# Kernel optimization log

Measured on AMD Instinct MI355X. Metric: run time of the kernel, lower is better.

## Reference

```python
import jax, jax.numpy as jnp
import numpy as np

ATT_DIM = 512
HEADS = 8
HEAD_DIM = ATT_DIM // HEADS
D_IN = 512
LEFT_MASK = 256
RIGHT_MASK = 0
LARGE = 1e30


def pos_encoding(S, d):
    # Transformer-XL sinusoid table over relative positions S-1 .. -(S-1), length 2S-1.
    inv_freq = (1.0 / (10000.0 ** (np.arange(0, d, 2.0) / d))).astype(np.float32)
    pos = jnp.arange(S - 1, -S, -1, dtype=jnp.float32)          # [2S-1]
    ang = pos[:, None] * jnp.asarray(inv_freq)[None, :]          # [2S-1, d/2]
    # concat([sin, cos], -1) on a trailing singleton -> interleaved sin/cos per frequency
    return jnp.stack([jnp.sin(ang), jnp.cos(ang)], axis=-1).reshape(2 * S - 1, d)


def rel_shift(x):
    # x: [B, N, S, 2S-1] -> [B, N, S, S] with out[i, j] = x[i, S-1 - i + j]
    B, N, S, L = x.shape
    x = jnp.pad(x, ((0, 0), (0, 0), (0, 0), (1, 0)))             # [B,N,S,L+1]
    x = x.reshape(B, N, L + 1, S)[:, :, 1:, :]                   # [B,N,L,S]
    x = x.reshape(B, N, S, L)
    return x[:, :, :, :S]


def setup_inputs() -> dict:
    key = jax.random.key(0)
    ks = jax.random.split(key, 9)
    B, S, D = 2, 2048, D_IN
    scale = 0.02
    return {
        "x": jax.random.normal(ks[0], (B, S, D), dtype=jnp.float32),
        "Wq": jax.random.normal(ks[1], (D, ATT_DIM), dtype=jnp.float32) * scale,
        "b_con": jax.random.normal(ks[2], (ATT_DIM,), dtype=jnp.float32) * scale,
        "b_rel": jax.random.normal(ks[3], (ATT_DIM,), dtype=jnp.float32) * scale,
        "Wk": jax.random.normal(ks[4], (D, ATT_DIM), dtype=jnp.float32) * scale,
        "Wkr": jax.random.normal(ks[5], (D_IN, ATT_DIM), dtype=jnp.float32) * scale,
        "Wv": jax.random.normal(ks[6], (D, ATT_DIM), dtype=jnp.float32) * scale,
        "bv": jax.random.normal(ks[7], (ATT_DIM,), dtype=jnp.float32) * scale,
        "x_len": jax.random.randint(ks[8], (B,), 1, S + 1).astype(jnp.int32),
    }


def reference(x, Wq, b_con, b_rel, Wk, Wkr, Wv, bv, x_len):
    B, S, D = x.shape
    N, Dh = HEADS, HEAD_DIM

    # content/relative query share the kernel (TiedDense) with separate biases
    q_lin = jnp.einsum('bsd,de->bse', x, Wq)
    q_con = (q_lin + b_con).reshape(B, S, N, Dh)
    q_rel = (q_lin + b_rel).reshape(B, S, N, Dh)
    k_con = jnp.einsum('bsd,de->bse', x, Wk).reshape(B, S, N, Dh)

    content_energy = jnp.einsum('bind,bjnd->bnij', q_con, k_con)  # [B,N,S,S]

    pos_emb = pos_encoding(S, D_IN)                               # [2S-1, D]
    k_rel = (pos_emb @ Wkr).reshape(2 * S - 1, N, Dh)
    relative_energy = jnp.einsum('bind,jnd->bnij', q_rel, k_rel)  # [B,N,S,2S-1]
    relative_energy = rel_shift(relative_energy)                  # [B,N,S,S]

    energy = (content_energy + relative_energy) / jnp.sqrt(jnp.float32(Dh))

    # sequence mask over keys (broadcast [B,1,1,S]) * banded mask (band_part)
    j = jnp.arange(S)
    seq_mask = (j[None, :] < x_len[:, None]).astype(jnp.float32)[:, None, None, :]
    i = jnp.arange(S)[:, None]
    band = ((i - j[None, :] <= LEFT_MASK) & (j[None, :] - i <= RIGHT_MASK)).astype(jnp.float32)
    mask = seq_mask * band[None, None, :, :]

    masked_energy = energy - (1.0 - mask) * LARGE
    attention = jax.nn.softmax(masked_energy, axis=-1)

    v = (jnp.einsum('bsd,de->bse', x, Wv) + bv).reshape(B, S, N, Dh)
    context = jnp.einsum('bnij,bjnd->bind', attention, v).reshape(B, S, N * Dh)
    return context
```

## Files before the change

### kernel.cpp

```cpp
#include <hip/hip_runtime.h>
#include <math.h>

#define S_ 2048
#define NH 8
#define DH 64
#define RSTRIDE 264
#define LP 72

typedef __attribute__((ext_vector_type(8))) short short8;
typedef __attribute__((ext_vector_type(4))) float f32x4;
typedef unsigned short ushort_t;

__device__ __forceinline__ short bf16r(float x) {
    union { float f; unsigned u; } v; v.f = x;
    unsigned r = v.u + 0x7fffu + ((v.u >> 16) & 1u);
    return (short)(r >> 16);
}
__device__ __forceinline__ float b2f(ushort_t h) {
    union { float f; unsigned u; } v; v.u = ((unsigned)h) << 16; return v.f;
}

__global__ __launch_bounds__(256) void prep_kernel(
    const float* __restrict__ Wq, const float* __restrict__ Wk,
    const float* __restrict__ Wv, const float* __restrict__ Wkr,
    ushort_t* __restrict__ WTq, ushort_t* __restrict__ WTk,
    ushort_t* __restrict__ WTv, ushort_t* __restrict__ WTkr,
    ushort_t* __restrict__ pos)
{
    const int widx = blockIdx.z;
    const int t = threadIdx.x;
    if (widx == 4) {
        const int base = blockIdx.y * 8 + blockIdx.x;
        const float C = -0.051905126482615036f;
        const int f = t;
#pragma unroll
        for (int rep = 0; rep < 6; ++rep) {
            const int r = base + rep * 64;
            unsigned pk = 0;
            if (r <= 256) {
                float ang = (float)r * exp2f(C * (float)f);
                unsigned s = (unsigned)(ushort_t)bf16r(sinf(ang));
                unsigned c = (unsigned)(ushort_t)bf16r(cosf(ang));
                pk = s | (c << 16);
            }
            ((unsigned*)pos)[(size_t)r * 256 + f] = pk;
        }
        return;
    }
    const float* W = (widx == 0) ? Wq : (widx == 1) ? Wk : (widx == 2) ? Wv : Wkr;
    ushort_t* WT   = (widx == 0) ? WTq : (widx == 1) ? WTk : (widx == 2) ? WTv : WTkr;
    const int k0 = blockIdx.x * 64, n0 = blockIdx.y * 64;
    __shared__ __align__(16) ushort_t T[64][72];
    const int srow = t >> 2, sc0 = (t & 3) * 16;
    const float* src = &W[(size_t)(k0 + srow) * 512 + n0 + sc0];
#pragma unroll
    for (int u = 0; u < 16; ++u) T[sc0 + u][srow] = (ushort_t)bf16r(src[u]);
    __syncthreads();
    ushort_t* dst = &WT[(size_t)(n0 + srow) * 512 + k0 + sc0];
    *(short8*)dst       = *(const short8*)&T[srow][sc0];
    *(short8*)(dst + 8) = *(const short8*)&T[srow][sc0 + 8];
}

__global__ __launch_bounds__(256) void qkv_gemm(
    const float* __restrict__ x,
    const ushort_t* __restrict__ WTq, const ushort_t* __restrict__ WTk,
    const ushort_t* __restrict__ WTv,
    const ushort_t* __restrict__ pos, const ushort_t* __restrict__ WTkr,
    const float* __restrict__ b_con, const float* __restrict__ b_rel,
    const float* __restrict__ bv,
    ushort_t* __restrict__ qcon, ushort_t* __restrict__ qrel,
    ushort_t* __restrict__ kout, ushort_t* __restrict__ vT,
    ushort_t* __restrict__ krel)
{
    const int widx = blockIdx.y >> 3;
    const int tid = threadIdx.x, lane = tid & 63, w = tid >> 6;
    const int quad = lane >> 4, l16 = lane & 15;

    __shared__ __align__(16) ushort_t A_lds[128][40];
    __shared__ __align__(16) ushort_t B_lds[64][40];

    f32x4 acc[2][4];
#pragma unroll
    for (int mt = 0; mt < 2; ++mt)
#pragma unroll
        for (int nt = 0; nt < 4; ++nt) acc[mt][nt] = (f32x4){0.f, 0.f, 0.f, 0.f};

    const int arow = tid >> 1, ak0 = (tid & 1) * 16;
    const int brow = tid >> 2, bk0 = (tid & 3) * 8;

    if (widx < 2) {
        const int m0 = blockIdx.x * 128;
        const int n0 = (blockIdx.y & 7) * 64;
        const ushort_t* WT = (widx == 0) ? WTq : WTk;

        for (int k0 = 0; k0 < 512; k0 += 32) {
            const float* xs = &x[(size_t)(m0 + arow) * 512 + k0 + ak0];
            ushort_t t16[16];
#pragma unroll
            for (int u = 0; u < 16; ++u) t16[u] = (ushort_t)bf16r(xs[u]);
            *(short8*)&A_lds[arow][ak0]     = *(short8*)&t16[0];
            *(short8*)&A_lds[arow][ak0 + 8] = *(short8*)&t16[8];
            *(short8*)&B_lds[brow][bk0] =
                *(const short8*)&WT[(size_t)(n0 + brow) * 512 + k0 + bk0];
            __syncthreads();
            short8 a0 = *(const short8*)&A_lds[w * 32 + l16][quad * 8];
            short8 a1 = *(const short8*)&A_lds[w * 32 + 16 + l16][quad * 8];
#pragma unroll
            for (int nt = 0; nt < 4; ++nt) {
                short8 bb = *(const short8*)&B_lds[nt * 16 + l16][quad * 8];
                acc[0][nt] = __builtin_amdgcn_mfma_f32_16x16x32_bf16(a0, bb, acc[0][nt], 0, 0, 0);
                acc[1][nt] = __builtin_amdgcn_mfma_f32_16x16x32_bf16(a1, bb, acc[1][nt], 0, 0, 0);
            }
            __syncthreads();
        }

#pragma unroll
        for (int nt = 0; nt < 4; ++nt) {
            const int col = n0 + nt * 16 + l16;
            float bc = 0.f, br = 0.f;
            if (widx == 0) { bc = b_con[col]; br = b_rel[col]; }
#pragma unroll
            for (int mt = 0; mt < 2; ++mt) {
#pragma unroll
                for (int reg = 0; reg < 4; ++reg) {
                    const size_t m = (size_t)(m0 + w * 32 + mt * 16 + quad * 4 + reg);
                    const float val = acc[mt][nt][reg];
                    if (widx == 0) {
                        qcon[m * 512 + col] = (ushort_t)bf16r((val + bc) * 0.125f);
                        qrel[m * 512 + col] = (ushort_t)bf16r((val + br) * 0.125f);
                    } else {
                        kout[m * 512 + col] = (ushort_t)bf16r(val);
                    }
                }
            }
        }
    } else if (widx == 2) {
        const int vb = (blockIdx.y & 7) * 32 + blockIdx.x;
        const int m0d = (vb & 3) * 128;
        const int n0j = (vb >> 2) * 64;

        for (int k0 = 0; k0 < 512; k0 += 32) {
            *(short8*)&A_lds[arow][ak0] =
                *(const short8*)&WTv[(size_t)(m0d + arow) * 512 + k0 + ak0];
            *(short8*)&A_lds[arow][ak0 + 8] =
                *(const short8*)&WTv[(size_t)(m0d + arow) * 512 + k0 + ak0 + 8];
            const float* xs = &x[(size_t)(n0j + brow) * 512 + k0 + bk0];
            ushort_t t8[8];
#pragma unroll
            for (int u = 0; u < 8; ++u) t8[u] = (ushort_t)bf16r(xs[u]);
            *(short8*)&B_lds[brow][bk0] = *(short8*)&t8[0];
            __syncthreads();
            short8 a0 = *(const short8*)&A_lds[w * 32 + l16][quad * 8];
            short8 a1 = *(const short8*)&A_lds[w * 32 + 16 + l16][quad * 8];
#pragma unroll
            for (int nt = 0; nt < 4; ++nt) {
                short8 bb = *(const short8*)&B_lds[nt * 16 + l16][quad * 8];
                acc[0][nt] = __builtin_amdgcn_mfma_f32_16x16x32_bf16(a0, bb, acc[0][nt], 0, 0, 0);
                acc[1][nt] = __builtin_amdgcn_mfma_f32_16x16x32_bf16(a1, bb, acc[1][nt], 0, 0, 0);
            }
            __syncthreads();
        }

        const int b = n0j >> 11;
#pragma unroll
        for (int mt = 0; mt < 2; ++mt) {
#pragma unroll
            for (int reg = 0; reg < 4; ++reg) {
                const int d = m0d + w * 32 + mt * 16 + quad * 4 + reg;
                const int n = d >> 6, dd = d & 63;
                const float bvv = bv[d];
#pragma unroll
                for (int nt = 0; nt < 4; ++nt) {
                    const int s = (n0j + nt * 16 + l16) & 2047;
                    vT[((size_t)((b * NH + n) * 64 + dd)) * 2048 + s] =
                        (ushort_t)bf16r(acc[mt][nt][reg] + bvv);
                }
            }
        }
    } else {
        if (blockIdx.x >= 24) return;
        const int m0 = (blockIdx.x >> 3) * 128;
        const int n0 = (blockIdx.x & 7) * 64;

        for (int k0 = 0; k0 < 512; k0 += 32) {
            const ushort_t* ps = &pos[(size_t)(m0 + arow) * 512 + k0 + ak0];
            *(short8*)&A_lds[arow][ak0]     = *(const short8*)ps;
            *(short8*)&A_lds[arow][ak0 + 8] = *(const short8*)(ps + 8);
            *(short8*)&B_lds[brow][bk0] =
                *(const short8*)&WTkr[(size_t)(n0 + brow) * 512 + k0 + bk0];
            __syncthreads();
            short8 a0 = *(const short8*)&A_lds[w * 32 + l16][quad * 8];
            short8 a1 = *(const short8*)&A_lds[w * 32 + 16 + l16][quad * 8];
#pragma unroll
            for (int nt = 0; nt < 4; ++nt) {
                short8 bb = *(const short8*)&B_lds[nt * 16 + l16][quad * 8];
                acc[0][nt] = __builtin_amdgcn_mfma_f32_16x16x32_bf16(a0, bb, acc[0][nt], 0, 0, 0);
                acc[1][nt] = __builtin_amdgcn_mfma_f32_16x16x32_bf16(a1, bb, acc[1][nt], 0, 0, 0);
            }
            __syncthreads();
        }

#pragma unroll
        for (int nt = 0; nt < 4; ++nt) {
            const int col = n0 + nt * 16 + l16;
#pragma unroll
            for (int mt = 0; mt < 2; ++mt)
#pragma unroll
                for (int reg = 0; reg < 4; ++reg) {
                    const size_t m = (size_t)(m0 + w * 32 + mt * 16 + quad * 4 + reg);
                    krel[m * 512 + col] = (ushort_t)bf16r(acc[mt][nt][reg]);
                }
        }
    }
}

__global__ __launch_bounds__(256) void rel_gemm(
    const ushort_t* __restrict__ qrel, const ushort_t* __restrict__ krel,
    const ushort_t* __restrict__ vT, ushort_t* __restrict__ R,
    float* __restrict__ vmean)
{
    const int tile = blockIdx.x, n = blockIdx.y, b = blockIdx.z;
    const int tid = threadIdx.x, lane = tid & 63, w = tid >> 6;
    const int quad = lane >> 4, l16 = lane & 15;

    __shared__ __align__(16) ushort_t A_lds[128][LP];
    __shared__ __align__(16) ushort_t B_lds[64][LP];

    if (tile == 16) {
        const int row = tid >> 2, seg = tid & 3;
        const ushort_t* src = &vT[((size_t)((b * NH + n) * 64 + row)) * 2048 + seg * 512];
        float sum = 0.f;
        for (int it = 0; it < 64; ++it) {
            short8 h = *(const short8*)(src + it * 8);
#pragma unroll
            for (int u = 0; u < 8; ++u) sum += b2f((ushort_t)h[u]);
        }
        float* scratch = (float*)A_lds;
        scratch[row * 4 + seg] = sum;
        __syncthreads();
        if (tid < 64) {
            float s = scratch[tid * 4] + scratch[tid * 4 + 1]
                    + scratch[tid * 4 + 2] + scratch[tid * 4 + 3];
            vmean[(size_t)b * 512 + n * 64 + tid] = s * (1.0f / (float)S_);
        }
        return;
    }

    const int i0 = tile * 128;
    {
        const int srow = tid >> 1, sc0 = (tid & 1) * 32;
        const ushort_t* src = &qrel[((size_t)b * S_ + i0 + srow) * 512 + n * 64 + sc0];
#pragma unroll
        for (int u = 0; u < 4; ++u)
            *(short8*)&A_lds[srow][sc0 + u * 8] = *(const short8*)(src + u * 8);
    }

    const size_t rbase = ((size_t)(b * NH + n) * S_ + i0) * RSTRIDE;
    const int srow2 = tid >> 2, sc2 = (tid & 3) * 16;

#pragma unroll 1
    for (int rc = 0; rc < 5; ++rc) {
        __syncthreads();
        {
            const ushort_t* src = &krel[(size_t)(rc * 64 + srow2) * 512 + n * 64 + sc2];
            *(short8*)&B_lds[srow2][sc2]     = *(const short8*)src;
            *(short8*)&B_lds[srow2][sc2 + 8] = *(const short8*)(src + 8);
        }
        __syncthreads();

        short8 a[2][2];
#pragma unroll
        for (int mt = 0; mt < 2; ++mt) {
            a[mt][0] = *(const short8*)&A_lds[w * 32 + mt * 16 + l16][quad * 8];
            a[mt][1] = *(const short8*)&A_lds[w * 32 + mt * 16 + l16][quad * 8 + 32];
        }
#pragma unroll
        for (int nt = 0; nt < 4; ++nt) {
            short8 b0 = *(const short8*)&B_lds[nt * 16 + l16][quad * 8];
            short8 b1 = *(const short8*)&B_lds[nt * 16 + l16][quad * 8 + 32];
            const int r = rc * 64 + nt * 16 + l16;
#pragma unroll
            for (int mt = 0; mt < 2; ++mt) {
                f32x4 s = (f32x4){0.f, 0.f, 0.f, 0.f};
                s = __builtin_amdgcn_mfma_f32_16x16x32_bf16(a[mt][0], b0, s, 0, 0, 0);
                s = __builtin_amdgcn_mfma_f32_16x16x32_bf16(a[mt][1], b1, s, 0, 0, 0);
                if (r < RSTRIDE) {
#pragma unroll
                    for (int reg = 0; reg < 4; ++reg) {
                        const int i = w * 32 + mt * 16 + quad * 4 + reg;
                        R[rbase + (size_t)i * RSTRIDE + r] = (ushort_t)bf16r(s[reg]);
                    }
                }
            }
        }
    }
}

__global__ __launch_bounds__(128) void attn_kernel(
    const ushort_t* __restrict__ qcon, const ushort_t* __restrict__ kbuf,
    const ushort_t* __restrict__ vT, const ushort_t* __restrict__ R,
    const float* __restrict__ vmean, const int* __restrict__ xlen_p,
    float* __restrict__ out)
{
    const int bx = blockIdx.x;
    const int tile = ((bx & 7) << 3) | (bx >> 3);
    const int n = blockIdx.y, b = blockIdx.z;
    const int i0 = tile * 32;
    const int tid = threadIdx.x, lane = tid & 63, w = tid >> 6;
    const int quad = lane >> 4, l16 = lane & 15;
    const int xlen = xlen_p[b];

    __shared__ __align__(16) ushort_t q_lds[32][LP];
    __shared__ __align__(16) ushort_t k_lds[64][LP];
    __shared__ __align__(16) ushort_t vT_lds[64][LP];
    __shared__ __align__(16) ushort_t p_lds[32][LP];

    {
        const int qr = tid >> 2, qc = (tid & 3) * 16;
        const ushort_t* src = &qcon[((size_t)b * S_ + i0 + qr) * 512 + n * 64 + qc];
        *(short8*)&q_lds[qr][qc]     = *(const short8*)src;
        *(short8*)&q_lds[qr][qc + 8] = *(const short8*)(src + 8);
    }

    f32x4 Oa[4];
#pragma unroll
    for (int nt = 0; nt < 4; ++nt) Oa[nt] = (f32x4){0.f, 0.f, 0.f, 0.f};
    float lpart[4] = {};

    const size_t rrowB = (size_t)(b * NH + n) * S_ * RSTRIDE;
    const size_t vTbase = (size_t)((b * NH + n) * 64) * 2048;
    const int srow = tid >> 1, sc0 = (tid & 1) * 32;
    const short8 z8 = {0, 0, 0, 0, 0, 0, 0, 0};

    short8 kr[4], vr[4], kn[4], vn[4];
    ushort_t rc_[16], rn_[16];

    auto issue = [&](int c, short8* kd, short8* vd, ushort_t* rd) {
        const int jc0 = i0 - 256 + c * 64;
        const int jg = jc0 + srow;
        const bool okk = (jg >= 0);
        const ushort_t* ks = &kbuf[((size_t)b * S_ + jg) * 512 + n * 64 + sc0];
        const ushort_t* vs = &vT[vTbase + (size_t)srow * 2048 + jc0 + sc0];
#pragma unroll
        for (int u = 0; u < 4; ++u) {
            kd[u] = okk ? *(const short8*)(ks + u * 8) : z8;
            const bool okv = (jc0 + sc0 + u * 8) >= 0;
            vd[u] = okv ? *(const short8*)(vs + u * 8) : z8;
        }
#pragma unroll
        for (int jt = 0; jt < 4; ++jt) {
#pragma unroll
            for (int reg = 0; reg < 4; ++reg) {
                const int i = i0 + w * 16 + quad * 4 + reg;
                const int j = jc0 + jt * 16 + l16;
                const int r = i - j;
                const bool valid = (j >= 0) && (j < xlen) && (r >= 0) && (r <= 256);
                rd[jt * 4 + reg] = valid ? R[rrowB + (size_t)i * RSTRIDE + r]
                                         : (ushort_t)0;
            }
        }
    };

    issue(0, kr, vr, rc_);

#pragma unroll 1
    for (int c = 0; c < 5; ++c) {
        const int jc0 = i0 - 256 + c * 64;
        __syncthreads();
#pragma unroll
        for (int u = 0; u < 4; ++u) {
            *(short8*)&k_lds[srow][sc0 + u * 8]  = kr[u];
            *(short8*)&vT_lds[srow][sc0 + u * 8] = vr[u];
        }
        if (c < 4) issue(c + 1, kn, vn, rn_);
        __syncthreads();

        short8 aq0 = *(const short8*)&q_lds[w * 16 + l16][quad * 8];
        short8 aq1 = *(const short8*)&q_lds[w * 16 + l16][quad * 8 + 32];
        f32x4 Sacc[4];
#pragma unroll
        for (int jt = 0; jt < 4; ++jt) {
            short8 bk0 = *(const short8*)&k_lds[jt * 16 + l16][quad * 8];
            short8 bk1 = *(const short8*)&k_lds[jt * 16 + l16][quad * 8 + 32];
            f32x4 s = (f32x4){0.f, 0.f, 0.f, 0.f};
            s = __builtin_amdgcn_mfma_f32_16x16x32_bf16(aq0, bk0, s, 0, 0, 0);
            s = __builtin_amdgcn_mfma_f32_16x16x32_bf16(aq1, bk1, s, 0, 0, 0);
            Sacc[jt] = s;
        }

#pragma unroll
        for (int jt = 0; jt < 4; ++jt) {
#pragma unroll
            for (int reg = 0; reg < 4; ++reg) {
                const int i = i0 + w * 16 + quad * 4 + reg;
                const int j = jc0 + jt * 16 + l16;
                const int r = i - j;
                const bool valid = (j >= 0) && (j < xlen) && (r >= 0) && (r <= 256);
                float e = valid ? __expf(Sacc[jt][reg] + b2f(rc_[jt * 4 + reg])) : 0.f;
                lpart[reg] += e;
                p_lds[w * 16 + quad * 4 + reg][jt * 16 + l16] = (ushort_t)bf16r(e);
            }
        }
        __syncthreads();

        short8 ap0 = *(const short8*)&p_lds[w * 16 + l16][quad * 8];
        short8 ap1 = *(const short8*)&p_lds[w * 16 + l16][quad * 8 + 32];
#pragma unroll
        for (int nt = 0; nt < 4; ++nt) {
            short8 bv0 = *(const short8*)&vT_lds[nt * 16 + l16][quad * 8];
            short8 bv1 = *(const short8*)&vT_lds[nt * 16 + l16][quad * 8 + 32];
            Oa[nt] = __builtin_amdgcn_mfma_f32_16x16x32_bf16(ap0, bv0, Oa[nt], 0, 0, 0);
            Oa[nt] = __builtin_amdgcn_mfma_f32_16x16x32_bf16(ap1, bv1, Oa[nt], 0, 0, 0);
        }

#pragma unroll
        for (int u = 0; u < 4; ++u) { kr[u] = kn[u]; vr[u] = vn[u]; }
#pragma unroll
        for (int u = 0; u < 16; ++u) rc_[u] = rn_[u];
    }

#pragma unroll
    for (int reg = 0; reg < 4; ++reg) {
#pragma unroll
        for (int off = 1; off < 16; off <<= 1)
            lpart[reg] += __shfl_xor(lpart[reg], off, 64);
    }

#pragma unroll
    for (int reg = 0; reg < 4; ++reg) {
        const int i = i0 + w * 16 + quad * 4 + reg;
        const bool dead = (i >= xlen + 256);
        const float linv = 1.0f / lpart[reg];
#pragma unroll
        for (int nt = 0; nt < 4; ++nt) {
            const int d = n * 64 + nt * 16 + l16;
            float val = dead ? vmean[(size_t)b * 512 + d] : Oa[nt][reg] * linv;
            out[((size_t)b * S_ + i) * 512 + d] = val;
        }
    }
}

extern "C" void kernel_launch(void* const* d_in, const int* in_sizes, int n_in,
                              void* d_out, int out_size, void* d_ws, size_t ws_size,
                              hipStream_t stream) {
    const float* x     = (const float*)d_in[0];
    const float* Wq    = (const float*)d_in[1];
    const float* b_con = (const float*)d_in[2];
    const float* b_rel = (const float*)d_in[3];
    const float* Wk    = (const float*)d_in[4];
    const float* Wkr   = (const float*)d_in[5];
    const float* Wv    = (const float*)d_in[6];
    const float* bv    = (const float*)d_in[7];
    const int*   xlen  = (const int*)d_in[8];
    float* out = (float*)d_out;

    float* ws = (float*)d_ws;
    float* vmean = ws;
    ushort_t* ub   = (ushort_t*)(vmean + 1024);
    ushort_t* R    = ub;
    ushort_t* qcon = R    + 8650752;
    ushort_t* kbuf = qcon + 2097152;
    ushort_t* vT   = kbuf + 2097152;
    ushort_t* qrel = vT   + 2097152;
    ushort_t* krel = qrel + 2097152;
    ushort_t* pos  = krel + 196608;
    ushort_t* WTq  = pos  + 196608;
    ushort_t* WTk  = WTq + 262144;
    ushort_t* WTv  = WTk + 262144;
    ushort_t* WTkr = WTv + 262144;

    prep_kernel<<<dim3(8, 8, 5), 256, 0, stream>>>(Wq, Wk, Wv, Wkr,
                                                   WTq, WTk, WTv, WTkr, pos);
    qkv_gemm<<<dim3(32, 25), 256, 0, stream>>>(x, WTq, WTk, WTv, pos, WTkr,
                                               b_con, b_rel, bv,
                                               qcon, qrel, kbuf, vT, krel);
    rel_gemm<<<dim3(17, 8, 2), 256, 0, stream>>>(qrel, krel, vT, R, vmean);
    attn_kernel<<<dim3(64, 8, 2), 128, 0, stream>>>(qcon, kbuf, vT, R, vmean,
                                                    xlen, out);
}
```

Measured before the change: 146.6 us.

## Fuse relative-position GEMM into attention kernel and compute value mean algebraically

Drops the separate rel_gemm kernel and its large global R buffer. Each attention block now computes its own 32x257 relative-energy band from qrel and krel into shared memory and reads it during softmax, instead of gathering scalars from global memory. The value mean used for fully masked rows is now computed as mean(x)·Wv + bv, with mean(x) produced in prep_kernel and the small GEMV run in spare qkv_gemm blocks. This cuts one launch and a large write/read round trip. In exchange the attention kernel does extra MFMA work and krel loads, uses more LDS (lower occupancy), and mean(x)·Wv in fp32 differs slightly from averaging the bf16 V values.

```diff
diff --git a/kernel.cpp b/kernel.cpp
--- a/kernel.cpp
+++ b/kernel.cpp
@@ -4,7 +4,6 @@
 #define S_ 2048
 #define NH 8
 #define DH 64
-#define RSTRIDE 264
 #define LP 72
 
 typedef __attribute__((ext_vector_type(8))) short short8;
@@ -21,14 +20,17 @@
 }
 
 __global__ __launch_bounds__(256) void prep_kernel(
+    const float* __restrict__ x,
     const float* __restrict__ Wq, const float* __restrict__ Wk,
     const float* __restrict__ Wv, const float* __restrict__ Wkr,
     ushort_t* __restrict__ WTq, ushort_t* __restrict__ WTk,
     ushort_t* __restrict__ WTv, ushort_t* __restrict__ WTkr,
-    ushort_t* __restrict__ pos)
+    ushort_t* __restrict__ pos, float* __restrict__ xbar)
 {
     const int widx = blockIdx.z;
     const int t = threadIdx.x;
+    __shared__ __align__(16) ushort_t T[64][72];
+
     if (widx == 4) {
         const int base = blockIdx.y * 8 + blockIdx.x;
         const float C = -0.051905126482615036f;
@@ -47,10 +49,24 @@
         }
         return;
     }
+    if (widx == 5) {
+        if (blockIdx.y >= 2) return;
+        const int b = blockIdx.y, e0 = blockIdx.x * 64;
+        const int el = t & 63, stripe = t >> 6;
+        const float* xs = &x[((size_t)b * S_ + stripe * 512) * 512 + e0 + el];
+        float sum = 0.f;
+        for (int s = 0; s < 512; ++s) sum += xs[(size_t)s * 512];
+        float* sc = (float*)T;
+        sc[stripe * 64 + el] = sum;
+        __syncthreads();
+        if (t < 64)
+            xbar[b * 512 + e0 + t] =
+                (sc[t] + sc[64 + t] + sc[128 + t] + sc[192 + t]) * (1.0f / 2048.f);
+        return;
+    }
     const float* W = (widx == 0) ? Wq : (widx == 1) ? Wk : (widx == 2) ? Wv : Wkr;
     ushort_t* WT   = (widx == 0) ? WTq : (widx == 1) ? WTk : (widx == 2) ? WTv : WTkr;
     const int k0 = blockIdx.x * 64, n0 = blockIdx.y * 64;
-    __shared__ __align__(16) ushort_t T[64][72];
     const int srow = t >> 2, sc0 = (t & 3) * 16;
     const float* src = &W[(size_t)(k0 + srow) * 512 + n0 + sc0];
 #pragma unroll
@@ -66,11 +82,12 @@
     const ushort_t* __restrict__ WTq, const ushort_t* __restrict__ WTk,
     const ushort_t* __restrict__ WTv,
     const ushort_t* __restrict__ pos, const ushort_t* __restrict__ WTkr,
+    const float* __restrict__ xbar,
     const float* __restrict__ b_con, const float* __restrict__ b_rel,
     const float* __restrict__ bv,
     ushort_t* __restrict__ qcon, ushort_t* __restrict__ qrel,
     ushort_t* __restrict__ kout, ushort_t* __restrict__ vT,
-    ushort_t* __restrict__ krel)
+    ushort_t* __restrict__ krel, float* __restrict__ vmean)
 {
     const int widx = blockIdx.y >> 3;
     const int tid = threadIdx.x, lane = tid & 63, w = tid >> 6;
@@ -177,8 +194,7 @@
                 }
             }
         }
-    } else {
-        if (blockIdx.x >= 24) return;
+    } else if (blockIdx.x < 24) {
         const int m0 = (blockIdx.x >> 3) * 128;
         const int n0 = (blockIdx.x & 7) * 64;
 
@@ -211,96 +227,40 @@
                     krel[m * 512 + col] = (ushort_t)bf16r(acc[mt][nt][reg]);
                 }
         }
-    }
-}
-
-__global__ __launch_bounds__(256) void rel_gemm(
-    const ushort_t* __restrict__ qrel, const ushort_t* __restrict__ krel,
-    const ushort_t* __restrict__ vT, ushort_t* __restrict__ R,
-    float* __restrict__ vmean)
-{
-    const int tile = blockIdx.x, n = blockIdx.y, b = blockIdx.z;
-    const int tid = threadIdx.x, lane = tid & 63, w = tid >> 6;
-    const int quad = lane >> 4, l16 = lane & 15;
-
-    __shared__ __align__(16) ushort_t A_lds[128][LP];
-    __shared__ __align__(16) ushort_t B_lds[64][LP];
-
-    if (tile == 16) {
-        const int row = tid >> 2, seg = tid & 3;
-        const ushort_t* src = &vT[((size_t)((b * NH + n) * 64 + row)) * 2048 + seg * 512];
-        float sum = 0.f;
-        for (int it = 0; it < 64; ++it) {
-            short8 h = *(const short8*)(src + it * 8);
-#pragma unroll
-            for (int u = 0; u < 8; ++u) sum += b2f((ushort_t)h[u]);
-        }
-        float* scratch = (float*)A_lds;
-        scratch[row * 4 + seg] = sum;
-        __syncthreads();
-        if (tid < 64) {
-            float s = scratch[tid * 4] + scratch[tid * 4 + 1]
-                    + scratch[tid * 4 + 2] + scratch[tid * 4 + 3];
-            vmean[(size_t)b * 512 + n * 64 + tid] = s * (1.0f / (float)S_);
-        }
-        return;
-    }
-
-    const int i0 = tile * 128;
-    {
-        const int srow = tid >> 1, sc0 = (tid & 1) * 32;
-        const ushort_t* src = &qrel[((size_t)b * S_ + i0 + srow) * 512 + n * 64 + sc0];
-#pragma unroll
-        for (int u = 0; u < 4; ++u)
-            *(short8*)&A_lds[srow][sc0 + u * 8] = *(const short8*)(src + u * 8);
-    }
-
-    const size_t rbase = ((size_t)(b * NH + n) * S_ + i0) * RSTRIDE;
-    const int srow2 = tid >> 2, sc2 = (tid & 3) * 16;
-
-#pragma unroll 1
-    for (int rc = 0; rc < 5; ++rc) {
-        __syncthreads();
-        {
-            const ushort_t* src = &krel[(size_t)(rc * 64 + srow2) * 512 + n * 64 + sc2];
-            *(short8*)&B_lds[srow2][sc2]     = *(const short8*)src;
-            *(short8*)&B_lds[srow2][sc2 + 8] = *(const short8*)(src + 8);
-        }
-        __syncthreads();
-
-        short8 a[2][2];
-#pragma unroll
-        for (int mt = 0; mt < 2; ++mt) {
-            a[mt][0] = *(const short8*)&A_lds[w * 32 + mt * 16 + l16][quad * 8];
-            a[mt][1] = *(const short8*)&A_lds[w * 32 + mt * 16 + l16][quad * 8 + 32];
-        }
-#pragma unroll
-        for (int nt = 0; nt < 4; ++nt) {
-            short8 b0 = *(const short8*)&B_lds[nt * 16 + l16][quad * 8];
-            short8 b1 = *(const short8*)&B_lds[nt * 16 + l16][quad * 8 + 32];
-            const int r = rc * 64 + nt * 16 + l16;
-#pragma unroll
-            for (int mt = 0; mt < 2; ++mt) {
-                f32x4 s = (f32x4){0.f, 0.f, 0.f, 0.f};
-                s = __builtin_amdgcn_mfma_f32_16x16x32_bf16(a[mt][0], b0, s, 0, 0, 0);
-                s = __builtin_amdgcn_mfma_f32_16x16x32_bf16(a[mt][1], b1, s, 0, 0, 0);
-                if (r < RSTRIDE) {
-#pragma unroll
-                    for (int reg = 0; reg < 4; ++reg) {
-                        const int i = w * 32 + mt * 16 + quad * 4 + reg;
-                        R[rbase + (size_t)i * RSTRIDE + r] = (ushort_t)bf16r(s[reg]);
-                    }
-                }
-            }
+    } else {
+        const int d0 = (blockIdx.x - 24) * 64;
+        const int dl = tid & 63, qtr = tid >> 6;
+        const ushort_t* wrow = &WTv[(size_t)(d0 + dl) * 512 + qtr * 128];
+        const float* xb0 = &xbar[qtr * 128];
+        const float* xb1 = &xbar[512 + qtr * 128];
+        float pa = 0.f, pb = 0.f;
+        for (int k8 = 0; k8 < 16; ++k8) {
+            short8 wv8 = *(const short8*)(wrow + k8 * 8);
+#pragma unroll
+            for (int u = 0; u < 8; ++u) {
+                float wv = b2f((ushort_t)wv8[u]);
+                pa += xb0[k8 * 8 + u] * wv;
+                pb += xb1[k8 * 8 + u] * wv;
+            }
+        }
+        float* sc = (float*)A_lds;
+        sc[(qtr * 64 + dl) * 2 + 0] = pa;
+        sc[(qtr * 64 + dl) * 2 + 1] = pb;
+        __syncthreads();
+        if (tid < 128) {
+            const int bb = tid >> 6, dd = tid & 63;
+            float s = sc[(dd) * 2 + bb] + sc[(64 + dd) * 2 + bb]
+                    + sc[(128 + dd) * 2 + bb] + sc[(192 + dd) * 2 + bb];
+            vmean[(size_t)bb * 512 + d0 + dd] = s + bv[d0 + dd];
         }
     }
 }
 
 __global__ __launch_bounds__(128) void attn_kernel(
-    const ushort_t* __restrict__ qcon, const ushort_t* __restrict__ kbuf,
-    const ushort_t* __restrict__ vT, const ushort_t* __restrict__ R,
-    const float* __restrict__ vmean, const int* __restrict__ xlen_p,
-    float* __restrict__ out)
+    const ushort_t* __restrict__ qcon, const ushort_t* __restrict__ qrel,
+    const ushort_t* __restrict__ krel, const ushort_t* __restrict__ kbuf,
+    const ushort_t* __restrict__ vT, const float* __restrict__ vmean,
+    const int* __restrict__ xlen_p, float* __restrict__ out)
 {
     const int bx = blockIdx.x;
     const int tile = ((bx & 7) << 3) | (bx >> 3);
@@ -314,12 +274,46 @@
     __shared__ __align__(16) ushort_t k_lds[64][LP];
     __shared__ __align__(16) ushort_t vT_lds[64][LP];
     __shared__ __align__(16) ushort_t p_lds[32][LP];
+    __shared__ __align__(16) ushort_t Rb[32][264];
 
     {
         const int qr = tid >> 2, qc = (tid & 3) * 16;
-        const ushort_t* src = &qcon[((size_t)b * S_ + i0 + qr) * 512 + n * 64 + qc];
-        *(short8*)&q_lds[qr][qc]     = *(const short8*)src;
-        *(short8*)&q_lds[qr][qc + 8] = *(const short8*)(src + 8);
+        const ushort_t* qs = &qcon[((size_t)b * S_ + i0 + qr) * 512 + n * 64 + qc];
+        const ushort_t* rs = &qrel[((size_t)b * S_ + i0 + qr) * 512 + n * 64 + qc];
+        *(short8*)&q_lds[qr][qc]     = *(const short8*)qs;
+        *(short8*)&q_lds[qr][qc + 8] = *(const short8*)(qs + 8);
+        *(short8*)&p_lds[qr][qc]     = *(const short8*)rs;
+        *(short8*)&p_lds[qr][qc + 8] = *(const short8*)(rs + 8);
+    }
+
+    const int srow = tid >> 1, sc0 = (tid & 1) * 32;
+
+#pragma unroll 1
+    for (int rc = 0; rc < 5; ++rc) {
+        __syncthreads();
+        {
+            const ushort_t* ksrc = &krel[(size_t)(rc * 64 + srow) * 512 + n * 64 + sc0];
+#pragma unroll
+            for (int u = 0; u < 4; ++u)
+                *(short8*)&k_lds[srow][sc0 + u * 8] = *(const short8*)(ksrc + u * 8);
+        }
+        __syncthreads();
+        short8 ar0 = *(const short8*)&p_lds[w * 16 + l16][quad * 8];
+        short8 ar1 = *(const short8*)&p_lds[w * 16 + l16][quad * 8 + 32];
+#pragma unroll
+        for (int nt = 0; nt < 4; ++nt) {
+            short8 bk0 = *(const short8*)&k_lds[nt * 16 + l16][quad * 8];
+            short8 bk1 = *(const short8*)&k_lds[nt * 16 + l16][quad * 8 + 32];
+            f32x4 s = (f32x4){0.f, 0.f, 0.f, 0.f};
+            s = __builtin_amdgcn_mfma_f32_16x16x32_bf16(ar0, bk0, s, 0, 0, 0);
+            s = __builtin_amdgcn_mfma_f32_16x16x32_bf16(ar1, bk1, s, 0, 0, 0);
+            const int r = rc * 64 + nt * 16 + l16;
+            if (r <= 256) {
+#pragma unroll
+                for (int reg = 0; reg < 4; ++reg)
+                    Rb[w * 16 + quad * 4 + reg][r] = (ushort_t)bf16r(s[reg]);
+            }
+        }
     }
 
     f32x4 Oa[4];
@@ -327,15 +321,12 @@
     for (int nt = 0; nt < 4; ++nt) Oa[nt] = (f32x4){0.f, 0.f, 0.f, 0.f};
     float lpart[4] = {};
 
-    const size_t rrowB = (size_t)(b * NH + n) * S_ * RSTRIDE;
     const size_t vTbase = (size_t)((b * NH + n) * 64) * 2048;
-    const int srow = tid >> 1, sc0 = (tid & 1) * 32;
     const short8 z8 = {0, 0, 0, 0, 0, 0, 0, 0};
 
     short8 kr[4], vr[4], kn[4], vn[4];
-    ushort_t rc_[16], rn_[16];
-
-    auto issue = [&](int c, short8* kd, short8* vd, ushort_t* rd) {
+
+    auto issue = [&](int c, short8* kd, short8* vd) {
         const int jc0 = i0 - 256 + c * 64;
         const int jg = jc0 + srow;
         const bool okk = (jg >= 0);
@@ -347,21 +338,9 @@
             const bool okv = (jc0 + sc0 + u * 8) >= 0;
             vd[u] = okv ? *(const short8*)(vs + u * 8) : z8;
         }
-#pragma unroll
-        for (int jt = 0; jt < 4; ++jt) {
-#pragma unroll
-            for (int reg = 0; reg < 4; ++reg) {
-                const int i = i0 + w * 16 + quad * 4 + reg;
-                const int j = jc0 + jt * 16 + l16;
-                const int r = i - j;
-                const bool valid = (j >= 0) && (j < xlen) && (r >= 0) && (r <= 256);
-                rd[jt * 4 + reg] = valid ? R[rrowB + (size_t)i * RSTRIDE + r]
-                                         : (ushort_t)0;
-            }
-        }
     };
 
-    issue(0, kr, vr, rc_);
+    issue(0, kr, vr);
 
 #pragma unroll 1
     for (int c = 0; c < 5; ++c) {
@@ -372,7 +351,7 @@
             *(short8*)&k_lds[srow][sc0 + u * 8]  = kr[u];
             *(short8*)&vT_lds[srow][sc0 + u * 8] = vr[u];
         }
-        if (c < 4) issue(c + 1, kn, vn, rn_);
+        if (c < 4) issue(c + 1, kn, vn);
         __syncthreads();
 
         short8 aq0 = *(const short8*)&q_lds[w * 16 + l16][quad * 8];
@@ -392,13 +371,16 @@
         for (int jt = 0; jt < 4; ++jt) {
 #pragma unroll
             for (int reg = 0; reg < 4; ++reg) {
-                const int i = i0 + w * 16 + quad * 4 + reg;
+                const int row = w * 16 + quad * 4 + reg;
+                const int i = i0 + row;
                 const int j = jc0 + jt * 16 + l16;
                 const int r = i - j;
                 const bool valid = (j >= 0) && (j < xlen) && (r >= 0) && (r <= 256);
-                float e = valid ? __expf(Sacc[jt][reg] + b2f(rc_[jt * 4 + reg])) : 0.f;
+                const int rcl = min(max(r, 0), 256);
+                float rvv = b2f(Rb[row][rcl]);
+                float e = valid ? __expf(Sacc[jt][reg] + rvv) : 0.f;
                 lpart[reg] += e;
-                p_lds[w * 16 + quad * 4 + reg][jt * 16 + l16] = (ushort_t)bf16r(e);
+                p_lds[row][jt * 16 + l16] = (ushort_t)bf16r(e);
             }
         }
         __syncthreads();
@@ -415,8 +397,6 @@
 
 #pragma unroll
         for (int u = 0; u < 4; ++u) { kr[u] = kn[u]; vr[u] = vn[u]; }
-#pragma unroll
-        for (int u = 0; u < 16; ++u) rc_[u] = rn_[u];
     }
 
 #pragma unroll
@@ -456,9 +436,9 @@
 
     float* ws = (float*)d_ws;
     float* vmean = ws;
-    ushort_t* ub   = (ushort_t*)(vmean + 1024);
-    ushort_t* R    = ub;
-    ushort_t* qcon = R    + 8650752;
+    float* xbar  = vmean + 1024;
+    ushort_t* ub   = (ushort_t*)(xbar + 1024);
+    ushort_t* qcon = ub;
     ushort_t* kbuf = qcon + 2097152;
     ushort_t* vT   = kbuf + 2097152;
     ushort_t* qrel = vT   + 2097152;
@@ -469,12 +449,11 @@
     ushort_t* WTv  = WTk + 262144;
     ushort_t* WTkr = WTv + 262144;
 
-    prep_kernel<<<dim3(8, 8, 5), 256, 0, stream>>>(Wq, Wk, Wv, Wkr,
-                                                   WTq, WTk, WTv, WTkr, pos);
-    qkv_gemm<<<dim3(32, 25), 256, 0, stream>>>(x, WTq, WTk, WTv, pos, WTkr,
+    prep_kernel<<<dim3(8, 8, 6), 256, 0, stream>>>(x, Wq, Wk, Wv, Wkr,
+                                                   WTq, WTk, WTv, WTkr, pos, xbar);
+    qkv_gemm<<<dim3(32, 25), 256, 0, stream>>>(x, WTq, WTk, WTv, pos, WTkr, xbar,
                                                b_con, b_rel, bv,
-                                               qcon, qrel, kbuf, vT, krel);
-    rel_gemm<<<dim3(17, 8, 2), 256, 0, stream>>>(qrel, krel, vT, R, vmean);
-    attn_kernel<<<dim3(64, 8, 2), 128, 0, stream>>>(qcon, kbuf, vT, R, vmean,
-                                                    xlen, out);
-}
+                                               qcon, qrel, kbuf, vT, krel, vmean);
+    attn_kernel<<<dim3(64, 8, 2), 128, 0, stream>>>(qcon, qrel, krel, kbuf, vT,
+                                                    vmean, xlen, out);
+}
```

Measured after the change: 160.2 us. 9.3% more time.
